# Optimization experiments

Hardware: AMD Instinct MI355X
Metric: run time of the kernel (lower is better)

## Reference

```python
import jax, jax.numpy as jnp
import numpy as np

E, TOPK = 32, 2            # hardcoded in LossMOEDecoder
D, HID, BOT, OUT = 768, 2048, 256, 768
B, S = 2, 128


def setup_inputs() -> dict:
    key = jax.random.key(0)
    ks = jax.random.split(key, 7)
    p = lambda k, shape: jax.random.normal(k, shape, dtype=jnp.float32) * 0.02
    return {
        "x": jax.random.normal(ks[0], (B, S, D), dtype=jnp.float32),
        "gate_w": p(ks[1], (E, D)),                 # MoEGate.weight
        "W1": p(ks[2], (E, D, HID)),  "b1": jnp.zeros((E, HID), jnp.float32),
        "W2": p(ks[3], (E, HID, HID)), "b2": jnp.zeros((E, HID), jnp.float32),
        "W3": p(ks[4], (E, HID, BOT)), "b3": jnp.zeros((E, BOT), jnp.float32),
        "Wl": p(ks[5], (E, BOT, OUT)), "bl": jnp.zeros((E, OUT), jnp.float32),
    }


def reference(x, gate_w, W1, b1, W2, b2, W3, b3, Wl, bl):
    Bz, Sl, d = x.shape
    xt = x.reshape(-1, d)                                    # [N, d] tokens
    # --- gate: softmax then top-k (values permutation-invariant vs torch sorted=False)
    scores = jax.nn.softmax(xt @ gate_w.T, axis=-1)          # [N, E]
    topk_w, topk_idx = jax.lax.top_k(scores, TOPK)           # [N, k]
    topk_w = topk_w / (topk_w.sum(-1, keepdims=True) + 1e-20)  # norm_topk_prob
    # --- experts: batched over the (small, fixed) expert axis; exact GELU as nn.GELU
    gelu = lambda v: jax.nn.gelu(v, approximate=False)
    h = gelu(jnp.einsum('nd,edh->enh', xt, W1) + b1[:, None, :])   # [E, N, HID]
    h = gelu(jnp.einsum('enh,ehg->eng', h, W2) + b2[:, None, :])   # [E, N, HID]
    z = jnp.einsum('eng,egb->enb', h, W3) + b3[:, None, :]         # [E, N, BOT]
    out_all = jnp.einsum('enb,ebo->eno', z, Wl) + bl[:, None, :]   # [E, N, OUT]
    # --- combine: gather each token's top-k expert outputs, weighted sum
    sel = jnp.take_along_axis(out_all.transpose(1, 0, 2),          # [N, E, OUT]
                              topk_idx[:, :, None], axis=1)        # [N, k, OUT]
    y = (sel * topk_w[:, :, None]).sum(axis=1)                     # [N, OUT]
    return y.reshape(Bz, Sl, OUT)
```

## Files before the change

### kernel.cpp

```cpp
#include <hip/hip_runtime.h>
#include <math.h>

#define NEXP 32
#define NTOK 256
#define DIMD 768
#define DHID 2048
#define DBOT 256
#define DOUT 768
#define NSLOT 512

__global__ __launch_bounds__(64) void gate_kernel(
    const float* __restrict__ x, const float* __restrict__ gw,
    int* __restrict__ topk_idx, float* __restrict__ topk_w) {
  const int n = blockIdx.x;
  const int l = threadIdx.x;
  const float* xr = x + n * DIMD;
  float xs[12];
#pragma unroll
  for (int j = 0; j < 12; j++) xs[j] = xr[l + 64 * j];
  float logit[NEXP];
#pragma unroll
  for (int e = 0; e < NEXP; e++) {
    const float* g = gw + e * DIMD;
    float p = 0.f;
#pragma unroll
    for (int j = 0; j < 12; j++) p = fmaf(xs[j], g[l + 64 * j], p);
#pragma unroll
    for (int m = 1; m < 64; m <<= 1) p += __shfl_xor(p, m);
    logit[e] = p;
  }
  int i0 = 0; float m0 = logit[0];
#pragma unroll
  for (int e = 1; e < NEXP; e++) { if (logit[e] > m0) { m0 = logit[e]; i0 = e; } }
  int i1 = -1; float m1 = -3.4e38f;
#pragma unroll
  for (int e = 0; e < NEXP; e++) { if (e != i0 && logit[e] > m1) { m1 = logit[e]; i1 = e; } }
  const float e1 = expf(m1 - m0);
  const float w0 = 1.f / (1.f + e1);
  const float w1 = e1 * w0;
  if (l == 0) {
    topk_idx[2 * n] = i0; topk_idx[2 * n + 1] = i1;
    topk_w[2 * n] = w0;  topk_w[2 * n + 1] = w1;
  }
}

__global__ __launch_bounds__(256) void build_lists(
    const int* __restrict__ topk_idx,
    int* __restrict__ counts, int* __restrict__ offsets,
    int* __restrict__ tok_list, int* __restrict__ tok2slot) {
  __shared__ int cnt[NEXP], base[NEXP], fill[NEXP];
  const int t = threadIdx.x;
  if (t < NEXP) { cnt[t] = 0; fill[t] = 0; }
  __syncthreads();
  const int e0 = topk_idx[2 * t], e1 = topk_idx[2 * t + 1];
  atomicAdd(&cnt[e0], 1);
  atomicAdd(&cnt[e1], 1);
  __syncthreads();
  if (t == 0) { int s = 0; for (int i = 0; i < NEXP; i++) { base[i] = s; s += cnt[i]; } }
  __syncthreads();
  const int p0 = atomicAdd(&fill[e0], 1);
  tok_list[base[e0] + p0] = t; tok2slot[2 * t] = base[e0] + p0;
  const int p1 = atomicAdd(&fill[e1], 1);
  tok_list[base[e1] + p1] = t; tok2slot[2 * t + 1] = base[e1] + p1;
  if (t < NEXP) { counts[t] = cnt[t]; offsets[t] = base[t]; }
}

__device__ __forceinline__ float gelu_f(float v) {
  return 0.5f * v * (1.f + erff(v * 0.70710678118654752f));
}

#define FMA4(A, XS, WV) \
  A.x = fmaf(XS, WV.x, A.x); A.y = fmaf(XS, WV.y, A.y); \
  A.z = fmaf(XS, WV.z, A.z); A.w = fmaf(XS, WV.w, A.w)

template <int MODE>
__global__ __launch_bounds__(512, 2) void ff_kernel(
    const float* __restrict__ Ain, const float* __restrict__ W,
    const float* __restrict__ Bias, float* __restrict__ Out,
    const float* __restrict__ zpart,
    const int* __restrict__ offsets, const int* __restrict__ counts,
    const int* __restrict__ tok_list) {
  constexpr int KBLK  = (MODE == 0) ? 768 : (MODE == 1) ? 2048 : 256;
  constexpr int NCT   = (MODE <= 1) ? 2048 : (MODE == 2) ? 256 : 768;
  constexpr int INS   = (MODE == 0) ? DIMD : DHID;
  constexpr int NSEC  = KBLK / 256;
  constexpr int COLT  = NCT / 256;
  constexpr int KFULL = (MODE == 2) ? DHID : KBLK;
  __shared__ float act_t[256 * 32];
  const int tid = threadIdx.x;
  const int tg  = tid >> 6;
  const int cg  = tid & 63;
  const int e   = blockIdx.y;
  const int ct  = blockIdx.x % COLT;
  const int kb  = blockIdx.x / COLT;
  const int cnt = counts[e];
  const int off = offsets[e];
  const int col = ct * 256 + cg * 4;
  const float* Wcol = W + ((size_t)e * KFULL + kb * 256) * NCT + col;
  const int tok = tid & 31;
  const int kk  = tid >> 5;

  for (int tc0 = 0; tc0 < cnt; tc0 += 32) {
    const int tcn = min(32, cnt - tc0);
    float4 acc[4];
#pragma unroll
    for (int t = 0; t < 4; t++) acc[t] = {0.f, 0.f, 0.f, 0.f};
    float4 wbuf[8];
#pragma unroll
    for (int d = 0; d < 4; d++) wbuf[d] = *(const float4*)(Wcol + (size_t)d * NCT);

    for (int s = 0; s < NSEC; s++) {
      __syncthreads();
      {
        float v[16];
        if (tok < tcn) {
          const int slot = off + tc0 + tok;
          if (MODE == 3) {
            const float* bs = Bias + (size_t)e * DBOT + kk * 16;
#pragma unroll
            for (int j = 0; j < 16; j += 4) {
              float4 q = *(const float4*)(bs + j);
#pragma unroll
              for (int k = 0; k < 8; k++) {
                const float4 p = *(const float4*)(
                    zpart + ((size_t)k * NSLOT + slot) * DBOT + kk * 16 + j);
                q.x += p.x; q.y += p.y; q.z += p.z; q.w += p.w;
              }
              v[j] = q.x; v[j + 1] = q.y; v[j + 2] = q.z; v[j + 3] = q.w;
            }
          } else {
            const int row = (MODE == 0) ? tok_list[slot] : slot;
            const float* src = Ain + (size_t)row * INS + kb * 256 + s * 256 + kk * 16;
#pragma unroll
            for (int j = 0; j < 16; j += 4) {
              const float4 q = *(const float4*)(src + j);
              v[j] = q.x; v[j + 1] = q.y; v[j + 2] = q.z; v[j + 3] = q.w;
            }
          }
        } else {
#pragma unroll
          for (int j = 0; j < 16; j++) v[j] = 0.f;
        }
#pragma unroll
        for (int j = 0; j < 16; j++) act_t[(kk * 16 + j) * 32 + tok] = v[j];
      }
      __syncthreads();

#pragma unroll 8
      for (int rr = 0; rr < 256; ++rr) {
        const int r   = s * 256 + rr;
        const int cur = rr & 7;
        const int pre = (rr + 4) & 7;
        const int rp  = min(r + 4, KBLK - 1);
        wbuf[pre] = *(const float4*)(Wcol + (size_t)rp * NCT);
        const float4 xv = *(const float4*)(&act_t[rr * 32 + tg * 4]);
        FMA4(acc[0], xv.x, wbuf[cur]);
        FMA4(acc[1], xv.y, wbuf[cur]);
        FMA4(acc[2], xv.z, wbuf[cur]);
        FMA4(acc[3], xv.w, wbuf[cur]);
      }
    }

    float4 bv = {0.f, 0.f, 0.f, 0.f};
    if (MODE <= 1) bv = *(const float4*)(Bias + (size_t)e * NCT + col);
#pragma unroll
    for (int tt = 0; tt < 4; tt++) {
      if (tg * 4 + tt < tcn) {
        const int slot = off + tc0 + tg * 4 + tt;
        float4 o = acc[tt];
        if (MODE <= 1) {
          o.x = gelu_f(o.x + bv.x); o.y = gelu_f(o.y + bv.y);
          o.z = gelu_f(o.z + bv.z); o.w = gelu_f(o.w + bv.w);
          *(float4*)(Out + (size_t)slot * NCT + col) = o;
        } else if (MODE == 2) {
          *(float4*)(Out + ((size_t)kb * NSLOT + slot) * DBOT + col) = o;
        } else {
          *(float4*)(Out + (size_t)slot * DOUT + col) = o;
        }
      }
    }
    __syncthreads();
  }
}

__global__ __launch_bounds__(192) void combine_kernel(
    const float* __restrict__ OutS, const float* __restrict__ bl,
    const int* __restrict__ topk_idx, const float* __restrict__ topk_w,
    const int* __restrict__ tok2slot, float* __restrict__ y) {
  const int n = blockIdx.x;
  const int c = threadIdx.x * 4;
  const int s0 = tok2slot[2 * n], s1 = tok2slot[2 * n + 1];
  const int e0 = topk_idx[2 * n], e1 = topk_idx[2 * n + 1];
  const float w0 = topk_w[2 * n], w1 = topk_w[2 * n + 1];
  const float4 a  = *(const float4*)(OutS + (size_t)s0 * DOUT + c);
  const float4 b  = *(const float4*)(OutS + (size_t)s1 * DOUT + c);
  const float4 ba = *(const float4*)(bl + (size_t)e0 * DOUT + c);
  const float4 bb = *(const float4*)(bl + (size_t)e1 * DOUT + c);
  float4 o;
  o.x = w0 * (a.x + ba.x) + w1 * (b.x + bb.x);
  o.y = w0 * (a.y + ba.y) + w1 * (b.y + bb.y);
  o.z = w0 * (a.z + ba.z) + w1 * (b.z + bb.z);
  o.w = w0 * (a.w + ba.w) + w1 * (b.w + bb.w);
  *(float4*)(y + (size_t)n * DOUT + c) = o;
}

extern "C" void kernel_launch(void* const* d_in, const int* in_sizes, int n_in,
                              void* d_out, int out_size, void* d_ws, size_t ws_size,
                              hipStream_t stream) {
  const float* x  = (const float*)d_in[0];
  const float* gw = (const float*)d_in[1];
  const float* W1 = (const float*)d_in[2];
  const float* b1 = (const float*)d_in[3];
  const float* W2 = (const float*)d_in[4];
  const float* b2 = (const float*)d_in[5];
  const float* W3 = (const float*)d_in[6];
  const float* b3 = (const float*)d_in[7];
  const float* Wl = (const float*)d_in[8];
  const float* bl = (const float*)d_in[9];
  float* y  = (float*)d_out;
  float* ws = (float*)d_ws;

  float* topk_w   = ws;
  int*   topk_idx = (int*)(ws + 512);
  int*   counts   = (int*)(ws + 1024);
  int*   offsets  = (int*)(ws + 1056);
  int*   tok_list = (int*)(ws + 1088);
  int*   tok2slot = (int*)(ws + 1600);
  float* B1    = ws + 4096;
  float* B2    = B1 + (size_t)NSLOT * DHID;
  float* zpart = B2 + (size_t)NSLOT * DHID;
  float* OutS  = zpart + (size_t)8 * NSLOT * DBOT;

  gate_kernel<<<NTOK, 64, 0, stream>>>(x, gw, topk_idx, topk_w);
  build_lists<<<1, 256, 0, stream>>>(topk_idx, counts, offsets, tok_list, tok2slot);
  ff_kernel<0><<<dim3(8, 32), 512, 0, stream>>>(x,  W1, b1, B1, nullptr,
                                                offsets, counts, tok_list);
  ff_kernel<1><<<dim3(8, 32), 512, 0, stream>>>(B1, W2, b2, B2, nullptr,
                                                offsets, counts, tok_list);
  ff_kernel<2><<<dim3(8, 32), 512, 0, stream>>>(B2, W3, nullptr, zpart, nullptr,
                                                offsets, counts, tok_list);
  ff_kernel<3><<<dim3(3, 32), 512, 0, stream>>>(nullptr, Wl, b3, OutS, zpart,
                                                offsets, counts, tok_list);
  combine_kernel<<<NTOK, 192, 0, stream>>>(OutS, bl, topk_idx, topk_w, tok2slot, y);
}
```

Before: 444.9 us.

## Stage expert weights through LDS with async double-buffered global_load_lds pipeline

New measurement: 401.4 us. -9.8%, faster.

```diff
diff --git a/kernel.cpp b/kernel.cpp
--- a/kernel.cpp
+++ b/kernel.cpp
@@ -47,7 +47,8 @@
 __global__ __launch_bounds__(256) void build_lists(
     const int* __restrict__ topk_idx,
     int* __restrict__ counts, int* __restrict__ offsets,
-    int* __restrict__ tok_list, int* __restrict__ tok2slot) {
+    int* __restrict__ tok_list, int* __restrict__ tok2slot,
+    int* __restrict__ slot_expert) {
   __shared__ int cnt[NEXP], base[NEXP], fill[NEXP];
   const int t = threadIdx.x;
   if (t < NEXP) { cnt[t] = 0; fill[t] = 0; }
@@ -60,13 +61,30 @@
   __syncthreads();
   const int p0 = atomicAdd(&fill[e0], 1);
   tok_list[base[e0] + p0] = t; tok2slot[2 * t] = base[e0] + p0;
+  slot_expert[base[e0] + p0] = e0;
   const int p1 = atomicAdd(&fill[e1], 1);
   tok_list[base[e1] + p1] = t; tok2slot[2 * t + 1] = base[e1] + p1;
+  slot_expert[base[e1] + p1] = e1;
   if (t < NEXP) { counts[t] = cnt[t]; offsets[t] = base[t]; }
 }
 
 __device__ __forceinline__ float gelu_f(float v) {
   return 0.5f * v * (1.f + erff(v * 0.70710678118654752f));
+}
+
+__global__ __launch_bounds__(64) void zsum_kernel(
+    const float* __restrict__ zpart, const float* __restrict__ b3,
+    const int* __restrict__ slot_expert, float* __restrict__ zsum) {
+  const int slot = blockIdx.x;
+  const int c = threadIdx.x * 4;
+  const int e = slot_expert[slot];
+  float4 q = *(const float4*)(b3 + (size_t)e * DBOT + c);
+#pragma unroll
+  for (int k = 0; k < 8; k++) {
+    const float4 p = *(const float4*)(zpart + ((size_t)k * NSLOT + slot) * DBOT + c);
+    q.x += p.x; q.y += p.y; q.z += p.z; q.w += p.w;
+  }
+  *(float4*)(zsum + (size_t)slot * DBOT + c) = q;
 }
 
 #define FMA4(A, XS, WV) \
@@ -77,88 +95,93 @@
 __global__ __launch_bounds__(512, 2) void ff_kernel(
     const float* __restrict__ Ain, const float* __restrict__ W,
     const float* __restrict__ Bias, float* __restrict__ Out,
-    const float* __restrict__ zpart,
     const int* __restrict__ offsets, const int* __restrict__ counts,
     const int* __restrict__ tok_list) {
-  constexpr int KBLK  = (MODE == 0) ? 768 : (MODE == 1) ? 2048 : 256;
   constexpr int NCT   = (MODE <= 1) ? 2048 : (MODE == 2) ? 256 : 768;
-  constexpr int INS   = (MODE == 0) ? DIMD : DHID;
-  constexpr int NSEC  = KBLK / 256;
-  constexpr int COLT  = NCT / 256;
-  constexpr int KFULL = (MODE == 2) ? DHID : KBLK;
-  __shared__ float act_t[256 * 32];
-  const int tid = threadIdx.x;
-  const int tg  = tid >> 6;
-  const int cg  = tid & 63;
-  const int e   = blockIdx.y;
-  const int ct  = blockIdx.x % COLT;
-  const int kb  = blockIdx.x / COLT;
+  constexpr int KFULL = (MODE == 0) ? 768 : (MODE == 3) ? 256 : 2048;
+  constexpr int INS   = (MODE == 0) ? DIMD : (MODE == 3) ? DBOT : DHID;
+  constexpr int NSEC  = (MODE == 0) ? 12 : (MODE == 1) ? 32 : 4;
+  __shared__ float Wlds[2 * 64 * 256];
+  __shared__ float act_t[2 * 64 * 32];
+  const int tid  = threadIdx.x;
+  const int lane = tid & 63;
+  const int wave = tid >> 6;
+  const int tg   = wave;
+  const int e    = blockIdx.y;
+  const int kb   = (MODE == 2) ? blockIdx.x : 0;
+  const int ct   = (MODE == 2) ? 0 : blockIdx.x;
+  const int kbase = kb * 256;
   const int cnt = counts[e];
   const int off = offsets[e];
-  const int col = ct * 256 + cg * 4;
-  const float* Wcol = W + ((size_t)e * KFULL + kb * 256) * NCT + col;
+  const int col = ct * 256 + lane * 4;
+  const float* Wsrc = W + ((size_t)e * KFULL) * NCT + (size_t)ct * 256;
   const int tok = tid & 31;
   const int kk  = tid >> 5;
 
   for (int tc0 = 0; tc0 < cnt; tc0 += 32) {
     const int tcn = min(32, cnt - tc0);
+    const int slot = off + tc0 + tok;
+    const float* Arow = nullptr;
+    if (tok < tcn) {
+      const int row = (MODE == 0) ? tok_list[slot] : slot;
+      Arow = Ain + (size_t)row * INS + kbase;
+    }
+
     float4 acc[4];
 #pragma unroll
     for (int t = 0; t < 4; t++) acc[t] = {0.f, 0.f, 0.f, 0.f};
-    float4 wbuf[8];
-#pragma unroll
-    for (int d = 0; d < 4; d++) wbuf[d] = *(const float4*)(Wcol + (size_t)d * NCT);
+    float4 av = {0.f, 0.f, 0.f, 0.f};
+
+    auto a_issue = [&](int s) {
+      if (Arow) av = *(const float4*)(Arow + s * 64 + kk * 4);
+      else      av = {0.f, 0.f, 0.f, 0.f};
+    };
+    auto w_issue = [&](int b, int s) {
+      float* wl = Wlds + b * 16384;
+      const float* src = Wsrc + (size_t)(kbase + s * 64) * NCT;
+#pragma unroll
+      for (int c = 0; c < 8; c++) {
+        const int r = c * 8 + wave;
+        __builtin_amdgcn_global_load_lds(
+            (const __attribute__((address_space(1))) void*)(src + (size_t)r * NCT + lane * 4),
+            (__attribute__((address_space(3))) void*)(wl + r * 256),
+            16, 0, 0);
+      }
+    };
+    auto a_write = [&](int b) {
+      float* at = act_t + b * 2048;
+      at[(kk * 4 + 0) * 32 + tok] = av.x;
+      at[(kk * 4 + 1) * 32 + tok] = av.y;
+      at[(kk * 4 + 2) * 32 + tok] = av.z;
+      at[(kk * 4 + 3) * 32 + tok] = av.w;
+    };
+
+    a_issue(0);
+    w_issue(0, 0);
+    a_write(0);
+    __syncthreads();
 
     for (int s = 0; s < NSEC; s++) {
+      const int b = s & 1;
+      if (s + 1 < NSEC) {
+        a_issue(s + 1);
+        w_issue(b ^ 1, s + 1);
+      }
+      {
+        const float* wl = Wlds + b * 16384 + lane * 4;
+        const float* at = act_t + b * 2048 + tg * 4;
+#pragma unroll 8
+        for (int r = 0; r < 64; r++) {
+          const float4 wv = *(const float4*)(wl + r * 256);
+          const float4 xv = *(const float4*)(at + r * 32);
+          FMA4(acc[0], xv.x, wv);
+          FMA4(acc[1], xv.y, wv);
+          FMA4(acc[2], xv.z, wv);
+          FMA4(acc[3], xv.w, wv);
+        }
+      }
+      if (s + 1 < NSEC) a_write(b ^ 1);
       __syncthreads();
-      {
-        float v[16];
-        if (tok < tcn) {
-          const int slot = off + tc0 + tok;
-          if (MODE == 3) {
-            const float* bs = Bias + (size_t)e * DBOT + kk * 16;
-#pragma unroll
-            for (int j = 0; j < 16; j += 4) {
-              float4 q = *(const float4*)(bs + j);
-#pragma unroll
-              for (int k = 0; k < 8; k++) {
-                const float4 p = *(const float4*)(
-                    zpart + ((size_t)k * NSLOT + slot) * DBOT + kk * 16 + j);
-                q.x += p.x; q.y += p.y; q.z += p.z; q.w += p.w;
-              }
-              v[j] = q.x; v[j + 1] = q.y; v[j + 2] = q.z; v[j + 3] = q.w;
-            }
-          } else {
-            const int row = (MODE == 0) ? tok_list[slot] : slot;
-            const float* src = Ain + (size_t)row * INS + kb * 256 + s * 256 + kk * 16;
-#pragma unroll
-            for (int j = 0; j < 16; j += 4) {
-              const float4 q = *(const float4*)(src + j);
-              v[j] = q.x; v[j + 1] = q.y; v[j + 2] = q.z; v[j + 3] = q.w;
-            }
-          }
-        } else {
-#pragma unroll
-          for (int j = 0; j < 16; j++) v[j] = 0.f;
-        }
-#pragma unroll
-        for (int j = 0; j < 16; j++) act_t[(kk * 16 + j) * 32 + tok] = v[j];
-      }
-      __syncthreads();
-
-#pragma unroll 8
-      for (int rr = 0; rr < 256; ++rr) {
-        const int r   = s * 256 + rr;
-        const int cur = rr & 7;
-        const int pre = (rr + 4) & 7;
-        const int rp  = min(r + 4, KBLK - 1);
-        wbuf[pre] = *(const float4*)(Wcol + (size_t)rp * NCT);
-        const float4 xv = *(const float4*)(&act_t[rr * 32 + tg * 4]);
-        FMA4(acc[0], xv.x, wbuf[cur]);
-        FMA4(acc[1], xv.y, wbuf[cur]);
-        FMA4(acc[2], xv.z, wbuf[cur]);
-        FMA4(acc[3], xv.w, wbuf[cur]);
-      }
     }
 
     float4 bv = {0.f, 0.f, 0.f, 0.f};
@@ -166,16 +189,16 @@
 #pragma unroll
     for (int tt = 0; tt < 4; tt++) {
       if (tg * 4 + tt < tcn) {
-        const int slot = off + tc0 + tg * 4 + tt;
+        const int os = off + tc0 + tg * 4 + tt;
         float4 o = acc[tt];
         if (MODE <= 1) {
           o.x = gelu_f(o.x + bv.x); o.y = gelu_f(o.y + bv.y);
           o.z = gelu_f(o.z + bv.z); o.w = gelu_f(o.w + bv.w);
-          *(float4*)(Out + (size_t)slot * NCT + col) = o;
+          *(float4*)(Out + (size_t)os * NCT + col) = o;
         } else if (MODE == 2) {
-          *(float4*)(Out + ((size_t)kb * NSLOT + slot) * DBOT + col) = o;
+          *(float4*)(Out + ((size_t)kb * NSLOT + os) * DBOT + col) = o;
         } else {
-          *(float4*)(Out + (size_t)slot * DOUT + col) = o;
+          *(float4*)(Out + (size_t)os * DOUT + col) = o;
         }
       }
     }
@@ -226,20 +249,19 @@
   int*   offsets  = (int*)(ws + 1056);
   int*   tok_list = (int*)(ws + 1088);
   int*   tok2slot = (int*)(ws + 1600);
+  int*   slot_exp = (int*)(ws + 2112);
   float* B1    = ws + 4096;
   float* B2    = B1 + (size_t)NSLOT * DHID;
   float* zpart = B2 + (size_t)NSLOT * DHID;
-  float* OutS  = zpart + (size_t)8 * NSLOT * DBOT;
+  float* zsum  = zpart + (size_t)8 * NSLOT * DBOT;
+  float* OutS  = zsum + (size_t)NSLOT * DBOT;
 
   gate_kernel<<<NTOK, 64, 0, stream>>>(x, gw, topk_idx, topk_w);
-  build_lists<<<1, 256, 0, stream>>>(topk_idx, counts, offsets, tok_list, tok2slot);
-  ff_kernel<0><<<dim3(8, 32), 512, 0, stream>>>(x,  W1, b1, B1, nullptr,
-                                                offsets, counts, tok_list);
-  ff_kernel<1><<<dim3(8, 32), 512, 0, stream>>>(B1, W2, b2, B2, nullptr,
-                                                offsets, counts, tok_list);
-  ff_kernel<2><<<dim3(8, 32), 512, 0, stream>>>(B2, W3, nullptr, zpart, nullptr,
-                                                offsets, counts, tok_list);
-  ff_kernel<3><<<dim3(3, 32), 512, 0, stream>>>(nullptr, Wl, b3, OutS, zpart,
-                                                offsets, counts, tok_list);
+  build_lists<<<1, 256, 0, stream>>>(topk_idx, counts, offsets, tok_list, tok2slot, slot_exp);
+  ff_kernel<0><<<dim3(8, 32), 512, 0, stream>>>(x,  W1, b1, B1, offsets, counts, tok_list);
+  ff_kernel<1><<<dim3(8, 32), 512, 0, stream>>>(B1, W2, b2, B2, offsets, counts, tok_list);
+  ff_kernel<2><<<dim3(8, 32), 512, 0, stream>>>(B2, W3, nullptr, zpart, offsets, counts, tok_list);
+  zsum_kernel<<<NSLOT, 64, 0, stream>>>(zpart, b3, slot_exp, zsum);
+  ff_kernel<3><<<dim3(3, 32), 512, 0, stream>>>(zsum, Wl, nullptr, OutS, offsets, counts, tok_list);
   combine_kernel<<<NTOK, 192, 0, stream>>>(OutS, bl, topk_idx, topk_w, tok2slot, y);
 }
```
